# Kernel tuning notes

Hardware: AMD Instinct MI355X
Metric: run time of the kernel (lower is better)

Reference implementation:

```python
import jax, jax.numpy as jnp
import numpy as np

TOP_K = 8          # n_activated_experts
ROUTE_SCALE = 2.5  # route_scale


def setup_inputs() -> dict:
    key = jax.random.key(0)
    k1, k2, k3 = jax.random.split(key, 3)
    T, D, E = 16384, 7168, 256
    x = jax.random.normal(k1, (T, D), dtype=jnp.float32)
    # nn.Linear weight layout: [out_features, in_features]
    W = jax.random.normal(k2, (E, D), dtype=jnp.float32) * (1.0 / np.sqrt(D))
    bias = jax.random.normal(k3, (E,), dtype=jnp.float32) * 0.01
    return {"x": x, "W": W, "bias": bias}


def reference(x, W, bias):
    # logits: [T, E] = x [T, D] @ W.T [D, E]
    logits = jnp.einsum("td,ed->te", x, W)
    scores = jax.nn.sigmoid(logits)              # original_scores
    biased = scores + bias                       # bias only affects expert selection
    _, indices = jax.lax.top_k(biased, TOP_K)    # [T, K] int32
    weights = jnp.take_along_axis(scores, indices, axis=-1)  # gather unbiased scores
    weights = weights / jnp.sum(weights, axis=-1, keepdims=True)  # sigmoid renorm
    weights = weights * ROUTE_SCALE
    return weights.astype(x.dtype), indices
```

## Files before the change

kernel.cpp:

```cpp
#include <hip/hip_runtime.h>
#include <cmath>

namespace {

typedef _Float16 half8 __attribute__((ext_vector_type(8)));
typedef float f32x4 __attribute__((ext_vector_type(4)));

constexpr int kTokens = 16384;
constexpr int kD      = 7168;
constexpr int kE      = 256;
constexpr int kTopK   = 8;
constexpr float kRouteScale = 2.5f;

constexpr int BM     = 32;
constexpr int BK     = 32;
constexpr int KSTEP  = 128;
constexpr int NT     = kD / BK;
constexpr int NSTEP  = kD / KSTEP;
constexpr float kS  = 4096.0f;
constexpr float kC  = 0.000244140625f;
constexpr size_t kWsTileB = 32768;
constexpr size_t kWsNeed  = (size_t)NT * kWsTileB;

__global__ void wconv_kernel(const float* __restrict__ W, unsigned char* __restrict__ ws)
{
    const int e = blockIdx.x;
    const int t = threadIdx.x;
    const float* src = W + (size_t)e * kD + (size_t)t * 8;
    float v[8];
    *reinterpret_cast<float4*>(v)     = *reinterpret_cast<const float4*>(src);
    *reinterpret_cast<float4*>(v + 4) = *reinterpret_cast<const float4*>(src + 4);
    half8 h, l;
#pragma unroll
    for (int j = 0; j < 8; ++j) {
        _Float16 hh = (_Float16)v[j];
        h[j] = hh;
        l[j] = (_Float16)((v[j] - (float)hh) * kS);
    }
    const int kt = t >> 2;
    const int kg = t & 3;
    const size_t off = (size_t)kt * kWsTileB +
                       (size_t)(((e >> 4) << 6) + (kg << 4) + (e & 15)) * 16;
    *reinterpret_cast<half8*>(ws + off)         = h;
    *reinterpret_cast<half8*>(ws + off + 16384) = l;
}

__global__ __launch_bounds__(512, 4)
void gate_mfma(const float* __restrict__ x,
               const unsigned char* __restrict__ wst,
               const float* __restrict__ bias,
               float* __restrict__ out)
{
    __shared__ unsigned char lds[32896];

    const int t    = threadIdx.x;
    const int lane = t & 63;
    const int wid  = t >> 6;
    const int m0   = blockIdx.x * BM;
    const int l15  = lane & 15;
    const int lg   = lane >> 4;

    const int srow = t >> 4;
    const int skc  = t & 15;
    const unsigned waddr = (unsigned)(((skc >> 2) << 12) + ((srow >> 4) << 10) +
                                      ((skc & 3) << 8) + ((((srow & 15) ^ skc) & 15) << 4));
    const float* xsrc = x + (size_t)(m0 + srow) * kD + (size_t)(skc * 8);

    const unsigned char* wb = wst + (size_t)(wid * 2) * 1024 + (size_t)lane * 16;

    f32x4 acc0[2][2], acc1[2][2], accL[2][2];
#pragma unroll
    for (int i = 0; i < 2; ++i)
#pragma unroll
        for (int j = 0; j < 2; ++j) {
            acc0[i][j] = f32x4{0.f,0.f,0.f,0.f};
            acc1[i][j] = f32x4{0.f,0.f,0.f,0.f};
            accL[i][j] = f32x4{0.f,0.f,0.f,0.f};
        }

    half8 bh[2][2];
    half8 bl[2];
    half8 axh[2][2];
    half8 axm[2][2];

    auto LOADBH = [&](int pp, int kt) {
        const unsigned char* p = wb + (size_t)kt * kWsTileB;
        bh[pp][0] = *reinterpret_cast<const half8*>(p);
        bh[pp][1] = *reinterpret_cast<const half8*>(p + 1024);
    };
    auto LOADBL = [&](int kt) {
        const unsigned char* p = wb + (size_t)kt * kWsTileB + 16384;
        bl[0] = *reinterpret_cast<const half8*>(p);
        bl[1] = *reinterpret_cast<const half8*>(p + 1024);
    };
    auto LDA = [&](int pp, unsigned bufc, int kk) {
        const unsigned base = bufc + (unsigned)(kk << 12) + (unsigned)(lg << 8) +
                              (unsigned)((((l15 ^ ((kk << 2) + lg)) & 15) << 4));
        axh[pp][0] = *reinterpret_cast<const half8*>(&lds[base]);
        axh[pp][1] = *reinterpret_cast<const half8*>(&lds[base + 1024]);
        axm[pp][0] = *reinterpret_cast<const half8*>(&lds[base + 2048]);
        axm[pp][1] = *reinterpret_cast<const half8*>(&lds[base + 3072]);
    };
    auto WRITESTEP = [&](unsigned base, const float4& a, const float4& b) {
        float v[8];
        *reinterpret_cast<float4*>(v)     = a;
        *reinterpret_cast<float4*>(v + 4) = b;
        half8 h0, h1;
#pragma unroll
        for (int j = 0; j < 8; ++j) {
            const _Float16 hh = (_Float16)v[j];
            h0[j] = hh;
            h1[j] = (_Float16)((v[j] - (float)hh) * kS);
        }
        *reinterpret_cast<half8*>(&lds[base + waddr])        = h0;
        *reinterpret_cast<half8*>(&lds[base + waddr + 2048]) = h1;
    };

    {
        float4 a = *reinterpret_cast<const float4*>(xsrc);
        float4 b = *reinterpret_cast<const float4*>(xsrc + 4);
        LOADBH(0, 0);
        WRITESTEP(0, a, b);
    }
    __syncthreads();

    for (int s = 0; s < NSTEP; ++s) {
        const unsigned bufc = (unsigned)((s & 1) << 14);
        const unsigned bufn = (unsigned)(((s + 1) & 1) << 14);
        const bool pre = (s + 1 < NSTEP);

        LDA(0, bufc, 0);
        float4 nv0{0,0,0,0}, nv1{0,0,0,0};
        if (pre) {
            const float* p = xsrc + (s + 1) * KSTEP;
            nv0 = *reinterpret_cast<const float4*>(p);
            nv1 = *reinterpret_cast<const float4*>(p + 4);
        }

#pragma unroll
        for (int kk = 0; kk < 4; ++kk) {
            const int kt = s * 4 + kk;
            LOADBL(kt);
            if (kk < 3) LDA((kk + 1) & 1, bufc, kk + 1);
            if (kt + 1 < NT) LOADBH((kk + 1) & 1, kt + 1);
            const int pp = kk & 1;
#pragma unroll
            for (int i = 0; i < 2; ++i)
#pragma unroll
                for (int j = 0; j < 2; ++j)
                    acc0[i][j] = __builtin_amdgcn_mfma_f32_16x16x32_f16(axh[pp][i], bh[pp][j], acc0[i][j], 0, 0, 0);
#pragma unroll
            for (int i = 0; i < 2; ++i)
#pragma unroll
                for (int j = 0; j < 2; ++j)
                    acc1[i][j] = __builtin_amdgcn_mfma_f32_16x16x32_f16(axm[pp][i], bh[pp][j], acc1[i][j], 0, 0, 0);
#pragma unroll
            for (int i = 0; i < 2; ++i)
#pragma unroll
                for (int j = 0; j < 2; ++j)
                    acc1[i][j] = __builtin_amdgcn_mfma_f32_16x16x32_f16(axh[pp][i], bl[j], acc1[i][j], 0, 0, 0);
        }

        if (pre) WRITESTEP(bufn, nv0, nv1);

        if (((s + 1) & 7) == 0) {
#pragma unroll
            for (int i = 0; i < 2; ++i)
#pragma unroll
                for (int j = 0; j < 2; ++j) {
                    accL[i][j] += acc0[i][j];
                    acc0[i][j] = f32x4{0.f,0.f,0.f,0.f};
                }
        }
        __syncthreads();
    }

    float (*sc)[257] = reinterpret_cast<float (*)[257]>(lds);
#pragma unroll
    for (int j = 0; j < 2; ++j) {
        const int col  = wid * 32 + j * 16 + l15;
        const float bv = bias[col];
#pragma unroll
        for (int i = 0; i < 2; ++i) {
            f32x4 z = (accL[i][j] + acc0[i][j]) + kC * acc1[i][j];
#pragma unroll
            for (int r = 0; r < 4; ++r) {
                const int row = i * 16 + lg * 4 + r;
                const float s = 1.0f / (1.0f + expf(-z[r]));
                sc[row][col] = s + bv;
            }
        }
    }
    __syncthreads();

    const int rr = t >> 4;
    const int g  = t & 15;

    float cval[kTopK];
    int   cidx[kTopK];

#pragma unroll
    for (int r = 0; r < kTopK; ++r) {
        float best = -INFINITY;
        int   bi   = kE;
        const float* rowp = sc[rr] + g * 16;
#pragma unroll 8
        for (int c = 0; c < 16; ++c) {
            const float v  = rowp[c];
            const int   ci = g * 16 + c;
            if (v > best || (v == best && ci < bi)) { best = v; bi = ci; }
        }
#pragma unroll
        for (int off = 8; off > 0; off >>= 1) {
            const float ov = __shfl_xor(best, off, 16);
            const int   oi = __shfl_xor(bi,   off, 16);
            if (ov > best || (ov == best && oi < bi)) { best = ov; bi = oi; }
        }
        cval[r] = best;
        cidx[r] = bi;
        if ((bi >> 4) == g) sc[rr][bi] = -INFINITY;
    }

    if (g == 0) {
        float uw[kTopK];
        float wsum = 0.0f;
#pragma unroll
        for (int r = 0; r < kTopK; ++r) {
            uw[r] = cval[r] - bias[cidx[r]];
            wsum += uw[r];
        }
        const float scale = kRouteScale / wsum;
        const size_t grow = (size_t)(m0 + rr);
#pragma unroll
        for (int r = 0; r < kTopK; ++r)
            out[grow * kTopK + r] = uw[r] * scale;
#pragma unroll
        for (int r = 0; r < kTopK; ++r)
            out[(size_t)kTokens * kTopK + grow * kTopK + r] = (float)cidx[r];
    }
}

constexpr int FBM = 32;
constexpr int FBK = 32;
constexpr int XS_STRIDE = 36;
constexpr int SC_STRIDE = 260;

__global__ __launch_bounds__(256, 2)
void gate_fused(const float* __restrict__ x,
                const float* __restrict__ W,
                const float* __restrict__ bias,
                float* __restrict__ out)
{
    __shared__ float smem[FBK * XS_STRIDE + FBK * kE];
    float (*xs)[XS_STRIDE] = reinterpret_cast<float (*)[XS_STRIDE]>(smem);
    float (*ws)[kE]        = reinterpret_cast<float (*)[kE]>(smem + FBK * XS_STRIDE);
    float (*sc)[SC_STRIDE] = reinterpret_cast<float (*)[SC_STRIDE]>(smem);

    const int t  = threadIdx.x;
    const int tx = t & 31;
    const int ty = t >> 5;
    const int m0 = blockIdx.x * FBM;
    const int lm = t >> 3;
    const int lc = t & 7;

    float acc[4][8];
    float cmp[4][8];
#pragma unroll
    for (int i = 0; i < 4; ++i)
#pragma unroll
        for (int j = 0; j < 8; ++j) { acc[i][j] = 0.0f; cmp[i][j] = 0.0f; }

    const float* xrow = x + (size_t)(m0 + lm) * kD;
    const float* wrow = W + (size_t)t * kD;

    for (int k0 = 0; k0 < kD; k0 += FBK) {
        float4 xv = *reinterpret_cast<const float4*>(xrow + k0 + 4 * lc);
        float4 wv[8];
#pragma unroll
        for (int i = 0; i < 8; ++i)
            wv[i] = *reinterpret_cast<const float4*>(wrow + k0 + 4 * i);
        __syncthreads();
        xs[4 * lc + 0][lm] = xv.x; xs[4 * lc + 1][lm] = xv.y;
        xs[4 * lc + 2][lm] = xv.z; xs[4 * lc + 3][lm] = xv.w;
#pragma unroll
        for (int i = 0; i < 8; ++i) {
            ws[4 * i + 0][t] = wv[i].x; ws[4 * i + 1][t] = wv[i].y;
            ws[4 * i + 2][t] = wv[i].z; ws[4 * i + 3][t] = wv[i].w;
        }
        __syncthreads();
        float p[4][8];
#pragma unroll
        for (int i = 0; i < 4; ++i)
#pragma unroll
            for (int j = 0; j < 8; ++j) p[i][j] = 0.0f;
#pragma unroll
        for (int k = 0; k < FBK; ++k) {
            float a[4], b[8];
            *reinterpret_cast<float4*>(a)     = *reinterpret_cast<const float4*>(&xs[k][4 * ty]);
            *reinterpret_cast<float4*>(b)     = *reinterpret_cast<const float4*>(&ws[k][4 * tx]);
            *reinterpret_cast<float4*>(b + 4) = *reinterpret_cast<const float4*>(&ws[k][128 + 4 * tx]);
#pragma unroll
            for (int i = 0; i < 4; ++i)
#pragma unroll
                for (int j = 0; j < 8; ++j)
                    p[i][j] = fmaf(a[i], b[j], p[i][j]);
        }
#pragma unroll
        for (int i = 0; i < 4; ++i)
#pragma unroll
            for (int j = 0; j < 8; ++j) {
                const float y = p[i][j] - cmp[i][j];
                const float s = acc[i][j] + y;
                cmp[i][j] = (s - acc[i][j]) - y;
                acc[i][j] = s;
            }
    }
    __syncthreads();
#pragma unroll
    for (int i = 0; i < 4; ++i) {
        const int row = 4 * ty + i;
#pragma unroll
        for (int j = 0; j < 8; ++j) {
            const int col = (j < 4) ? (4 * tx + j) : (128 + 4 * tx + (j - 4));
            const float s = 1.0f / (1.0f + expf(-acc[i][j]));
            sc[row][col] = s + bias[col];
        }
    }
    __syncthreads();
    const int rr = t >> 3;
    const int g  = t & 7;
    float cval[kTopK];
    int   cidx[kTopK];
#pragma unroll
    for (int r = 0; r < kTopK; ++r) {
        float best = -INFINITY;
        int   bi   = kE;
        const float* rowp = sc[rr] + g * 32;
#pragma unroll 8
        for (int c = 0; c < 32; ++c) {
            const float v  = rowp[c];
            const int   ci = g * 32 + c;
            if (v > best || (v == best && ci < bi)) { best = v; bi = ci; }
        }
#pragma unroll
        for (int off = 4; off > 0; off >>= 1) {
            const float ov = __shfl_xor(best, off, 8);
            const int   oi = __shfl_xor(bi,   off, 8);
            if (ov > best || (ov == best && oi < bi)) { best = ov; bi = oi; }
        }
        cval[r] = best; cidx[r] = bi;
        if ((bi >> 5) == g) sc[rr][bi] = -INFINITY;
        __syncthreads();
    }
    if (g == 0) {
        float uw[kTopK];
        float wsum = 0.0f;
#pragma unroll
        for (int r = 0; r < kTopK; ++r) { uw[r] = cval[r] - bias[cidx[r]]; wsum += uw[r]; }
        const float scale = kRouteScale / wsum;
        const size_t grow = (size_t)(m0 + rr);
#pragma unroll
        for (int r = 0; r < kTopK; ++r) out[grow * kTopK + r] = uw[r] * scale;
#pragma unroll
        for (int r = 0; r < kTopK; ++r)
            out[(size_t)kTokens * kTopK + grow * kTopK + r] = (float)cidx[r];
    }
}

}

extern "C" void kernel_launch(void* const* d_in, const int* in_sizes, int n_in,
                              void* d_out, int out_size, void* d_ws, size_t ws_size,
                              hipStream_t stream)
{
    const float* x    = (const float*)d_in[0];
    const float* W    = (const float*)d_in[1];
    const float* bias = (const float*)d_in[2];
    float* out = (float*)d_out;

    if (ws_size >= kWsNeed) {
        unsigned char* ws = (unsigned char*)d_ws;
        hipLaunchKernelGGL(wconv_kernel, dim3(kE), dim3(kD / 8), 0, stream, W, ws);
        hipLaunchKernelGGL(gate_mfma, dim3(kTokens / BM), dim3(512), 0, stream, x, ws, bias, out);
    } else {
        hipLaunchKernelGGL(gate_fused, dim3(kTokens / FBM), dim3(256), 0, stream, x, W, bias, out);
    }
}
```

Measured before the change: 256.6 us.

## Double the row tile to 64 with 16 waves and staggered K order

Each block now covers 64 tokens with 1024 threads arranged as 2 row groups × 8 column groups, so each staged W tile serves twice as many rows. Each wave starts its K sub-iteration at a different offset (kk0), which spreads W-tile fetches and LDS reads across waves. It also raises MFMA issue priority with s_setprio. The register double-buffered A-fragment prefetch is dropped in favour of direct LDS loads each sub-step, and the doubled LDS footprint (about 64 KB) can cut the number of resident blocks per CU.

```diff
diff --git a/kernel.cpp b/kernel.cpp
--- a/kernel.cpp
+++ b/kernel.cpp
@@ -12,7 +12,7 @@
 constexpr int kTopK   = 8;
 constexpr float kRouteScale = 2.5f;
 
-constexpr int BM     = 32;
+constexpr int BM     = 64;
 constexpr int BK     = 32;
 constexpr int KSTEP  = 128;
 constexpr int NT     = kD / BK;
@@ -45,28 +45,31 @@
     *reinterpret_cast<half8*>(ws + off + 16384) = l;
 }
 
-__global__ __launch_bounds__(512, 4)
+__global__ __launch_bounds__(1024, 4)
 void gate_mfma(const float* __restrict__ x,
                const unsigned char* __restrict__ wst,
                const float* __restrict__ bias,
                float* __restrict__ out)
 {
-    __shared__ unsigned char lds[32896];
+    __shared__ unsigned char lds[65792];
 
     const int t    = threadIdx.x;
     const int lane = t & 63;
-    const int wid  = t >> 6;
+    const int w    = t >> 6;
+    const int cg   = w >> 1;
+    const int rg   = w & 1;
+    const int kk0  = cg & 3;
     const int m0   = blockIdx.x * BM;
     const int l15  = lane & 15;
     const int lg   = lane >> 4;
 
     const int srow = t >> 4;
     const int skc  = t & 15;
-    const unsigned waddr = (unsigned)(((skc >> 2) << 12) + ((srow >> 4) << 10) +
+    const unsigned waddr = (unsigned)(((skc >> 2) << 13) + ((srow >> 4) << 10) +
                                       ((skc & 3) << 8) + ((((srow & 15) ^ skc) & 15) << 4));
     const float* xsrc = x + (size_t)(m0 + srow) * kD + (size_t)(skc * 8);
 
-    const unsigned char* wb = wst + (size_t)(wid * 2) * 1024 + (size_t)lane * 16;
+    const unsigned char* wb = wst + (size_t)(cg * 2) * 1024 + (size_t)lane * 16;
 
     f32x4 acc0[2][2], acc1[2][2], accL[2][2];
 #pragma unroll
@@ -80,8 +83,6 @@
 
     half8 bh[2][2];
     half8 bl[2];
-    half8 axh[2][2];
-    half8 axm[2][2];
 
     auto LOADBH = [&](int pp, int kt) {
         const unsigned char* p = wb + (size_t)kt * kWsTileB;
@@ -93,14 +94,6 @@
         bl[0] = *reinterpret_cast<const half8*>(p);
         bl[1] = *reinterpret_cast<const half8*>(p + 1024);
     };
-    auto LDA = [&](int pp, unsigned bufc, int kk) {
-        const unsigned base = bufc + (unsigned)(kk << 12) + (unsigned)(lg << 8) +
-                              (unsigned)((((l15 ^ ((kk << 2) + lg)) & 15) << 4));
-        axh[pp][0] = *reinterpret_cast<const half8*>(&lds[base]);
-        axh[pp][1] = *reinterpret_cast<const half8*>(&lds[base + 1024]);
-        axm[pp][0] = *reinterpret_cast<const half8*>(&lds[base + 2048]);
-        axm[pp][1] = *reinterpret_cast<const half8*>(&lds[base + 3072]);
-    };
     auto WRITESTEP = [&](unsigned base, const float4& a, const float4& b) {
         float v[8];
         *reinterpret_cast<float4*>(v)     = a;
@@ -113,23 +106,21 @@
             h1[j] = (_Float16)((v[j] - (float)hh) * kS);
         }
         *reinterpret_cast<half8*>(&lds[base + waddr])        = h0;
-        *reinterpret_cast<half8*>(&lds[base + waddr + 2048]) = h1;
+        *reinterpret_cast<half8*>(&lds[base + waddr + 4096]) = h1;
     };
 
     {
         float4 a = *reinterpret_cast<const float4*>(xsrc);
         float4 b = *reinterpret_cast<const float4*>(xsrc + 4);
-        LOADBH(0, 0);
+        LOADBH(0, kk0);
         WRITESTEP(0, a, b);
     }
     __syncthreads();
 
     for (int s = 0; s < NSTEP; ++s) {
-        const unsigned bufc = (unsigned)((s & 1) << 14);
-        const unsigned bufn = (unsigned)(((s + 1) & 1) << 14);
+        const unsigned bufc = (unsigned)((s & 1) << 15);
+        const unsigned bufn = (unsigned)(((s + 1) & 1) << 15);
         const bool pre = (s + 1 < NSTEP);
-
-        LDA(0, bufc, 0);
         float4 nv0{0,0,0,0}, nv1{0,0,0,0};
         if (pre) {
             const float* p = xsrc + (s + 1) * KSTEP;
@@ -138,27 +129,42 @@
         }
 
 #pragma unroll
-        for (int kk = 0; kk < 4; ++kk) {
+        for (int n = 0; n < 4; ++n) {
+            const int kk = (kk0 + n) & 3;
             const int kt = s * 4 + kk;
             LOADBL(kt);
-            if (kk < 3) LDA((kk + 1) & 1, bufc, kk + 1);
-            if (kt + 1 < NT) LOADBH((kk + 1) & 1, kt + 1);
-            const int pp = kk & 1;
+            const int kt_next = (n < 3) ? (s * 4 + ((kk0 + n + 1) & 3))
+                                        : ((s + 1) * 4 + kk0);
+            if (kt_next < NT) LOADBH((n & 1) ^ 1, kt_next);
+
+            half8 xh[2], xm[2];
+#pragma unroll
+            for (int i = 0; i < 2; ++i) {
+                const int rf = rg * 2 + i;
+                const unsigned base = bufc + (unsigned)(kk << 13) + (unsigned)(rf << 10) +
+                                      (unsigned)(lg << 8) +
+                                      (unsigned)((((l15 ^ ((kk << 2) + lg)) & 15) << 4));
+                xh[i] = *reinterpret_cast<const half8*>(&lds[base]);
+                xm[i] = *reinterpret_cast<const half8*>(&lds[base + 4096]);
+            }
+
+            __builtin_amdgcn_s_setprio(1);
 #pragma unroll
             for (int i = 0; i < 2; ++i)
 #pragma unroll
                 for (int j = 0; j < 2; ++j)
-                    acc0[i][j] = __builtin_amdgcn_mfma_f32_16x16x32_f16(axh[pp][i], bh[pp][j], acc0[i][j], 0, 0, 0);
+                    acc0[i][j] = __builtin_amdgcn_mfma_f32_16x16x32_f16(xh[i], bh[n & 1][j], acc0[i][j], 0, 0, 0);
 #pragma unroll
             for (int i = 0; i < 2; ++i)
 #pragma unroll
                 for (int j = 0; j < 2; ++j)
-                    acc1[i][j] = __builtin_amdgcn_mfma_f32_16x16x32_f16(axm[pp][i], bh[pp][j], acc1[i][j], 0, 0, 0);
+                    acc1[i][j] = __builtin_amdgcn_mfma_f32_16x16x32_f16(xm[i], bh[n & 1][j], acc1[i][j], 0, 0, 0);
 #pragma unroll
             for (int i = 0; i < 2; ++i)
 #pragma unroll
                 for (int j = 0; j < 2; ++j)
-                    acc1[i][j] = __builtin_amdgcn_mfma_f32_16x16x32_f16(axh[pp][i], bl[j], acc1[i][j], 0, 0, 0);
+                    acc1[i][j] = __builtin_amdgcn_mfma_f32_16x16x32_f16(xh[i], bl[j], acc1[i][j], 0, 0, 0);
+            __builtin_amdgcn_s_setprio(0);
         }
 
         if (pre) WRITESTEP(bufn, nv0, nv1);
@@ -178,16 +184,16 @@
     float (*sc)[257] = reinterpret_cast<float (*)[257]>(lds);
 #pragma unroll
     for (int j = 0; j < 2; ++j) {
-        const int col  = wid * 32 + j * 16 + l15;
+        const int col  = cg * 32 + j * 16 + l15;
         const float bv = bias[col];
 #pragma unroll
         for (int i = 0; i < 2; ++i) {
             f32x4 z = (accL[i][j] + acc0[i][j]) + kC * acc1[i][j];
 #pragma unroll
             for (int r = 0; r < 4; ++r) {
-                const int row = i * 16 + lg * 4 + r;
-                const float s = 1.0f / (1.0f + expf(-z[r]));
-                sc[row][col] = s + bv;
+                const int row = rg * 32 + i * 16 + lg * 4 + r;
+                const float sg = 1.0f / (1.0f + expf(-z[r]));
+                sc[row][col] = sg + bv;
             }
         }
     }
@@ -381,7 +387,7 @@
     if (ws_size >= kWsNeed) {
         unsigned char* ws = (unsigned char*)d_ws;
         hipLaunchKernelGGL(wconv_kernel, dim3(kE), dim3(kD / 8), 0, stream, W, ws);
-        hipLaunchKernelGGL(gate_mfma, dim3(kTokens / BM), dim3(512), 0, stream, x, ws, bias, out);
+        hipLaunchKernelGGL(gate_mfma, dim3(kTokens / BM), dim3(1024), 0, stream, x, ws, bias, out);
     } else {
         hipLaunchKernelGGL(gate_fused, dim3(kTokens / FBM), dim3(256), 0, stream, x, W, bias, out);
     }
```

Result: slower. 264.9 us (+3.2%).
